# Performance work log

Measured on AMD Instinct MI355X. Metric: run time of the kernel, lower is better.

## Reference

```python
import jax, jax.numpy as jnp
import numpy as np

HEADS = 8
OUT_C = 8
NEG_SLOPE = 0.2  # PyG GATConv default


def setup_inputs() -> dict:
    key = jax.random.key(0)
    k = jax.random.split(key, 6)
    N, F, E = 100000, 128, 1600000
    x = jax.random.normal(k[0], (N, F), dtype=jnp.float32)
    edge_index = jax.random.randint(k[1], (2, E), 0, N, dtype=jnp.int64)
    W = jax.random.normal(k[2], (F, HEADS * OUT_C), dtype=jnp.float32) * (1.0 / np.sqrt(F))
    att_src = jax.random.normal(k[3], (HEADS, OUT_C), dtype=jnp.float32) * 0.1
    att_dst = jax.random.normal(k[4], (HEADS, OUT_C), dtype=jnp.float32) * 0.1
    bias = jnp.zeros((HEADS * OUT_C,), dtype=jnp.float32)
    return {"x": x, "edge_index": edge_index, "W": W,
            "att_src": att_src, "att_dst": att_dst, "bias": bias}


def reference(x, edge_index, W, att_src, att_dst, bias):
    N = x.shape[0]
    # add self loops (PyG default add_self_loops=True)
    loops = jnp.arange(N, dtype=edge_index.dtype)
    src = jnp.concatenate([edge_index[0], loops])  # [E']
    dst = jnp.concatenate([edge_index[1], loops])  # [E']

    h = (x @ W).reshape(N, HEADS, OUT_C)          # [N,H,C]
    a_src = jnp.einsum('nhc,hc->nh', h, att_src)  # [N,H]
    a_dst = jnp.einsum('nhc,hc->nh', h, att_dst)  # [N,H]

    # per-edge LeakyReLU attention logits
    e = jax.nn.leaky_relu(a_src[src] + a_dst[dst], NEG_SLOPE)  # [E',H]

    # segment softmax over incoming edges of each destination node
    emax = jax.ops.segment_max(e, dst, num_segments=N)  # every node has a self loop
    ex = jnp.exp(e - emax[dst])
    denom = jax.ops.segment_sum(ex, dst, num_segments=N)
    alpha = ex / denom[dst]  # [E',H]  (dropout on alpha skipped: eval mode)

    # scatter-add weighted source features
    out = jax.ops.segment_sum(alpha[:, :, None] * h[src], dst, num_segments=N)  # [N,H,C]
    return out.reshape(N, HEADS * OUT_C) + bias
```

## Files before the change

kernel.cpp:

```cpp
#include <hip/hip_runtime.h>
#include <hip/hip_bf16.h>


#define F 128
#define HC 64
#define H 8
#define NSLC 64

__device__ inline ushort f2bf(float f) {
    unsigned u = __float_as_uint(f);
    u += 0x7fff + ((u >> 16) & 1);
    return (ushort)(u >> 16);
}

__global__ __launch_bounds__(256) void k_gemm(const float* __restrict__ x,
                                              const float* __restrict__ W,
                                              const float* __restrict__ att_src,
                                              const float* __restrict__ att_dst,
                                              ushort* __restrict__ h2,
                                              float* __restrict__ a_src,
                                              float* __restrict__ a_dst, int N) {
    __shared__ float xs[64][F];
    const int tid  = threadIdx.x;
    const int row0 = blockIdx.x * 64;
    #pragma unroll
    for (int i = 0; i < 8; ++i) {
        int idx = i * 256 + tid;
        int r = idx >> 5;
        float4 v = make_float4(0.f, 0.f, 0.f, 0.f);
        if (row0 + r < N) v = ((const float4*)x)[(size_t)row0 * 32 + idx];
        ((float4*)xs)[idx] = v;
    }
    __syncthreads();
    const int c0 = (tid & 15) * 4;
    const int r0 = (tid >> 4) * 4;
    float acc[4][4] = {};
    for (int k = 0; k < F; k += 4) {
        float w[4][4];
        *(float4*)w[0] = *(const float4*)&W[(size_t)(k + 0) * HC + c0];
        *(float4*)w[1] = *(const float4*)&W[(size_t)(k + 1) * HC + c0];
        *(float4*)w[2] = *(const float4*)&W[(size_t)(k + 2) * HC + c0];
        *(float4*)w[3] = *(const float4*)&W[(size_t)(k + 3) * HC + c0];
        #pragma unroll
        for (int i = 0; i < 4; ++i) {
            float4 xv = *(const float4*)&xs[r0 + i][k];
            #pragma unroll
            for (int c = 0; c < 4; ++c) {
                acc[i][c] += xv.x * w[0][c];
                acc[i][c] += xv.y * w[1][c];
                acc[i][c] += xv.z * w[2][c];
                acc[i][c] += xv.w * w[3][c];
            }
        }
    }
    const int head = (tid & 15) >> 1;
    const int cb   = c0 & 7;
    float as4[4], ad4[4];
    #pragma unroll
    for (int c = 0; c < 4; ++c) {
        as4[c] = att_src[head * 8 + cb + c];
        ad4[c] = att_dst[head * 8 + cb + c];
    }
    #pragma unroll
    for (int i = 0; i < 4; ++i) {
        int r = row0 + r0 + i;
        if (r < N) {
            ushort4 pk;
            pk.x = f2bf(acc[i][0]); pk.y = f2bf(acc[i][1]);
            pk.z = f2bf(acc[i][2]); pk.w = f2bf(acc[i][3]);
            *(ushort4*)&h2[(size_t)r * HC + c0] = pk;
            float ps = acc[i][0]*as4[0] + acc[i][1]*as4[1] +
                       acc[i][2]*as4[2] + acc[i][3]*as4[3];
            float pd = acc[i][0]*ad4[0] + acc[i][1]*ad4[1] +
                       acc[i][2]*ad4[2] + acc[i][3]*ad4[3];
            ps += __shfl_xor(ps, 1);
            pd += __shfl_xor(pd, 1);
            if ((tid & 1) == 0) {
                a_src[(size_t)r * H + head] = ps;
                a_dst[(size_t)r * H + head] = pd;
            }
        }
    }
}

__global__ __launch_bounds__(1024) void k_h(const int* __restrict__ ei,
                                            ushort* __restrict__ hist,
                                            int E, int npg) {
    extern __shared__ int lcnt[];
    const int grp = blockIdx.x & 7;
    const int lo  = grp * npg;
    const unsigned len = (unsigned)npg;
    for (int i = threadIdx.x; i < npg; i += 1024) lcnt[i] = 0;
    __syncthreads();
    const int t    = (blockIdx.x >> 3) * 1024 + threadIdx.x;
    const int nthr = (gridDim.x >> 3) * 1024;
    const int a0 = (4 - (E & 3)) & 3;
    const int nv = (E - a0) >> 2;
    const int4* vd = (const int4*)(ei + E + a0);
    for (int q = t; q < nv; q += nthr) {
        int4 d = vd[q];
        unsigned c;
        c = (unsigned)(d.x - lo); if (c < len) atomicAdd(&lcnt[c], 1);
        c = (unsigned)(d.y - lo); if (c < len) atomicAdd(&lcnt[c], 1);
        c = (unsigned)(d.z - lo); if (c < len) atomicAdd(&lcnt[c], 1);
        c = (unsigned)(d.w - lo); if (c < len) atomicAdd(&lcnt[c], 1);
    }
    if (blockIdx.x < 8) {
        int r = (E - a0) & 3;
        int e = -1;
        int tx = (int)threadIdx.x;
        if (tx < a0) e = tx;
        else if (tx - a0 < r) e = a0 + (nv << 2) + (tx - a0);
        if (e >= 0) {
            unsigned c = (unsigned)(ei[E + e] - lo);
            if (c < len) atomicAdd(&lcnt[c], 1);
        }
    }
    __syncthreads();
    ushort* hrow = hist + (size_t)blockIdx.x * npg;
    for (int i = threadIdx.x; i < npg; i += 1024) hrow[i] = (ushort)lcnt[i];
}

__global__ __launch_bounds__(256) void k_scan1(const ushort* __restrict__ hist,
                                               int* __restrict__ offs,
                                               int* __restrict__ bsums,
                                               int N, int npg) {
    __shared__ int s[256];
    int i = blockIdx.x * 256 + threadIdx.x;
    int v = 0;
    if (i < N) {
        int g = i / npg;
        int c = i - g * npg;
        const ushort* hp = hist + (size_t)g * npg + c;
        #pragma unroll 8
        for (int j = 0; j < NSLC; ++j) v += hp[(size_t)(j << 3) * npg];
        v += 1;
    }
    s[threadIdx.x] = v;
    __syncthreads();
    for (int d = 1; d < 256; d <<= 1) {
        int t = (threadIdx.x >= d) ? s[threadIdx.x - d] : 0;
        __syncthreads();
        s[threadIdx.x] += t;
        __syncthreads();
    }
    if (i < N) offs[i] = s[threadIdx.x] - v;
    if (threadIdx.x == 255) bsums[blockIdx.x] = s[255];
}

__global__ __launch_bounds__(512) void k_scan2(int* __restrict__ bsums, int nb) {
    __shared__ int s[512];
    int v = (threadIdx.x < nb) ? bsums[threadIdx.x] : 0;
    s[threadIdx.x] = v;
    __syncthreads();
    for (int d = 1; d < 512; d <<= 1) {
        int t = (threadIdx.x >= d) ? s[threadIdx.x - d] : 0;
        __syncthreads();
        s[threadIdx.x] += t;
        __syncthreads();
    }
    if (threadIdx.x < nb) bsums[threadIdx.x] = s[threadIdx.x] - v;
}

__global__ __launch_bounds__(256) void k_scan3(int* __restrict__ offs,
                                               const int* __restrict__ bsums,
                                               ushort* __restrict__ hist,
                                               int* __restrict__ srcs,
                                               int N, int npg, int Etot) {
    int i = blockIdx.x * 256 + threadIdx.x;
    if (i == 0) offs[N] = Etot;
    if (i >= N) return;
    int o = offs[i] + bsums[i >> 8];
    offs[i] = o;
    srcs[o] = i;
    int g = i / npg;
    int c = i - g * npg;
    ushort* hp = hist + (size_t)g * npg + c;
    int p = 0;
    #pragma unroll 8
    for (int j = 0; j < NSLC; ++j) {
        size_t off = (size_t)(j << 3) * npg;
        int t = hp[off];
        hp[off] = (ushort)p;
        p += t;
    }
}

__global__ __launch_bounds__(1024) void k_scat(const int* __restrict__ ei,
                                               const ushort* __restrict__ hist,
                                               const int* __restrict__ offs,
                                               int* __restrict__ srcs,
                                               int E, int npg) {
    extern __shared__ int lpos[];
    const int grp = blockIdx.x & 7;
    const int lo  = grp * npg;
    const unsigned len = (unsigned)npg;
    const ushort* hrow = hist + (size_t)blockIdx.x * npg;
    for (int i = threadIdx.x; i < npg; i += 1024)
        lpos[i] = offs[lo + i] + 1 + (int)hrow[i];
    __syncthreads();
    const int t    = (blockIdx.x >> 3) * 1024 + threadIdx.x;
    const int nthr = (gridDim.x >> 3) * 1024;
    const int a0 = (4 - (E & 3)) & 3;
    const int nv = (E - a0) >> 2;
    const int4* vd = (const int4*)(ei + E + a0);
    for (int q = t; q < nv; q += nthr) {
        int4 d = vd[q];
        unsigned c0 = (unsigned)(d.x - lo), c1 = (unsigned)(d.y - lo),
                 c2 = (unsigned)(d.z - lo), c3 = (unsigned)(d.w - lo);
        if ((c0 < len) | (c1 < len) | (c2 < len) | (c3 < len)) {
            int e = a0 + (q << 2);
            if (c0 < len) { int p = atomicAdd(&lpos[c0], 1); srcs[p] = ei[e];     }
            if (c1 < len) { int p = atomicAdd(&lpos[c1], 1); srcs[p] = ei[e + 1]; }
            if (c2 < len) { int p = atomicAdd(&lpos[c2], 1); srcs[p] = ei[e + 2]; }
            if (c3 < len) { int p = atomicAdd(&lpos[c3], 1); srcs[p] = ei[e + 3]; }
        }
    }
    if (blockIdx.x < 8) {
        int r = (E - a0) & 3;
        int e = -1;
        int tx = (int)threadIdx.x;
        if (tx < a0) e = tx;
        else if (tx - a0 < r) e = a0 + (nv << 2) + (tx - a0);
        if (e >= 0) {
            unsigned c = (unsigned)(ei[E + e] - lo);
            if (c < len) { int p = atomicAdd(&lpos[c], 1); srcs[p] = ei[e]; }
        }
    }
}

__global__ __launch_bounds__(256) void k_gat(const int* __restrict__ offs,
                                             const int* __restrict__ srcs,
                                             const ushort* __restrict__ h2,
                                             const float* __restrict__ a_src,
                                             const float* __restrict__ a_dst,
                                             const float* __restrict__ bias,
                                             float* __restrict__ out, int N) {
    const int lane = threadIdx.x & 63;
    const int half = lane >> 5;
    const int l32  = lane & 31;
    const int g    = l32 >> 3;
    const int hd   = l32 & 7;
    const int wave = threadIdx.x >> 6;
    const int d = blockIdx.x * 8 + wave * 2 + half;
    const bool valid = d < N;

    int off = 0, end = 0;
    float adst = 0.f;
    if (valid) {
        off  = offs[d];
        end  = offs[d + 1];
        adst = a_dst[d * H + hd];
    }

    float acc[8] = {0.f, 0.f, 0.f, 0.f, 0.f, 0.f, 0.f, 0.f};
    float den = 0.f;

    for (int i = off + g; i < end; i += 8) {
        const int i2 = i + 4;
        const bool has1 = (i2 < end);
        int s0 = srcs[i];
        int s1 = has1 ? srcs[i2] : s0;
        float a0 = a_src[s0 * H + hd] + adst;
        float a1 = a_src[s1 * H + hd] + adst;
        a0 = a0 > 0.f ? a0 : 0.2f * a0;
        a1 = a1 > 0.f ? a1 : 0.2f * a1;
        float ex0 = __expf(a0);
        float ex1 = has1 ? __expf(a1) : 0.f;
        uint4 u0 = *(const uint4*)(h2 + ((size_t)s0 << 6) + (hd << 3));
        uint4 u1 = *(const uint4*)(h2 + ((size_t)s1 << 6) + (hd << 3));
        acc[0] += ex0 * __uint_as_float(u0.x << 16);
        acc[1] += ex0 * __uint_as_float(u0.x & 0xffff0000u);
        acc[2] += ex0 * __uint_as_float(u0.y << 16);
        acc[3] += ex0 * __uint_as_float(u0.y & 0xffff0000u);
        acc[4] += ex0 * __uint_as_float(u0.z << 16);
        acc[5] += ex0 * __uint_as_float(u0.z & 0xffff0000u);
        acc[6] += ex0 * __uint_as_float(u0.w << 16);
        acc[7] += ex0 * __uint_as_float(u0.w & 0xffff0000u);
        acc[0] += ex1 * __uint_as_float(u1.x << 16);
        acc[1] += ex1 * __uint_as_float(u1.x & 0xffff0000u);
        acc[2] += ex1 * __uint_as_float(u1.y << 16);
        acc[3] += ex1 * __uint_as_float(u1.y & 0xffff0000u);
        acc[4] += ex1 * __uint_as_float(u1.z << 16);
        acc[5] += ex1 * __uint_as_float(u1.z & 0xffff0000u);
        acc[6] += ex1 * __uint_as_float(u1.w << 16);
        acc[7] += ex1 * __uint_as_float(u1.w & 0xffff0000u);
        den += ex0 + ex1;
    }

    #pragma unroll
    for (int m = 8; m <= 16; m <<= 1) {
        #pragma unroll
        for (int c = 0; c < 8; ++c) acc[c] += __shfl_xor(acc[c], m);
        den += __shfl_xor(den, m);
    }

    if (g == 0 && valid) {
        float r = 1.f / den;
        float4 o0, o1;
        o0.x = acc[0]*r + bias[hd*8+0]; o0.y = acc[1]*r + bias[hd*8+1];
        o0.z = acc[2]*r + bias[hd*8+2]; o0.w = acc[3]*r + bias[hd*8+3];
        o1.x = acc[4]*r + bias[hd*8+4]; o1.y = acc[5]*r + bias[hd*8+5];
        o1.z = acc[6]*r + bias[hd*8+6]; o1.w = acc[7]*r + bias[hd*8+7];
        *(float4*)&out[(size_t)d * HC + hd * 8]     = o0;
        *(float4*)&out[(size_t)d * HC + hd * 8 + 4] = o1;
    }
}

extern "C" void kernel_launch(void* const* d_in, const int* in_sizes, int n_in,
                              void* d_out, int out_size, void* d_ws, size_t ws_size,
                              hipStream_t stream) {
    const float* x       = (const float*)d_in[0];
    const int*   ei      = (const int*)d_in[1];
    const float* W       = (const float*)d_in[2];
    const float* att_src = (const float*)d_in[3];
    const float* att_dst = (const float*)d_in[4];
    const float* bias    = (const float*)d_in[5];
    const int N = in_sizes[0] / F;
    const int E = in_sizes[1] / 2;
    const int Etot = E + N;
    const int npg = (N + 7) / 8;
    float* out = (float*)d_out;

    ushort* h2    = (ushort*)d_ws;
    float*  a_src = (float*)(h2 + (size_t)N * HC);
    float*  a_dst = a_src + (size_t)N * H;
    int*    offs  = (int*)(a_dst + (size_t)N * H);
    int*    bsums = offs + N + 1;
    ushort* hist  = (ushort*)(bsums + 512);
    int*    srcs  = (int*)(hist + (size_t)8 * NSLC * npg);

    const int nb = (N + 255) / 256;
    const size_t ldsz = (size_t)npg * sizeof(int);
    k_gemm <<<(N + 63) / 64, 256, 0, stream>>>(x, W, att_src, att_dst, h2, a_src, a_dst, N);
    k_h    <<<8 * NSLC, 1024, ldsz, stream>>>(ei, hist, E, npg);
    k_scan1<<<nb, 256, 0, stream>>>(hist, offs, bsums, N, npg);
    k_scan2<<<1, 512, 0, stream>>>(bsums, nb);
    k_scan3<<<nb, 256, 0, stream>>>(offs, bsums, hist, srcs, N, npg, Etot);
    k_scat <<<8 * NSLC, 1024, ldsz, stream>>>(ei, hist, offs, srcs, E, npg);
    k_gat  <<<(N + 7) / 8, 256, 0, stream>>>(offs, srcs, h2, a_src, a_dst, bias, out, N);
}
```

Measured before the change: 237.8 us.

## Pre-partition edges by destination group into packed payload before CSR histogram and scatter

Previously the histogram and scatter kernels each made every one of 8 group-blocks stream the entire destination array and filter for its own group, reading edge_index eight times over. The new path first counts edges per coarse destination group, scans those counts, and writes a packed (src<<14 | local dst) payload grouped by destination range. The histogram and scatter kernels then read only their own group's slice, and the slice count is halved. This adds three small kernels and an extra payload buffer. The packing assumes src fits in 18 bits and a local destination index fits in 14 bits, which holds for N=100000.

```diff
diff --git a/kernel.cpp b/kernel.cpp
--- a/kernel.cpp
+++ b/kernel.cpp
@@ -5,7 +5,8 @@
 #define F 128
 #define HC 64
 #define H 8
-#define NSLC 64
+#define NS 32
+#define PB 512
 
 __device__ inline ushort f2bf(float f) {
     unsigned u = __float_as_uint(f);
@@ -83,39 +84,121 @@
     }
 }
 
-__global__ __launch_bounds__(1024) void k_h(const int* __restrict__ ei,
-                                            ushort* __restrict__ hist,
-                                            int E, int npg) {
-    extern __shared__ int lcnt[];
-    const int grp = blockIdx.x & 7;
-    const int lo  = grp * npg;
-    const unsigned len = (unsigned)npg;
-    for (int i = threadIdx.x; i < npg; i += 1024) lcnt[i] = 0;
-    __syncthreads();
-    const int t    = (blockIdx.x >> 3) * 1024 + threadIdx.x;
-    const int nthr = (gridDim.x >> 3) * 1024;
+__device__ inline unsigned grp_of(int d, unsigned Mg) {
+    return (unsigned)(((unsigned long long)(unsigned)d * Mg) >> 32);
+}
+
+__global__ __launch_bounds__(256) void k_c(const int* __restrict__ ei,
+                                           int* __restrict__ pcntT,
+                                           int E, unsigned Mg) {
+    __shared__ int cnt[8];
+    if (threadIdx.x < 8) cnt[threadIdx.x] = 0;
+    __syncthreads();
+    const int t    = blockIdx.x * 256 + threadIdx.x;
+    const int nthr = PB * 256;
     const int a0 = (4 - (E & 3)) & 3;
     const int nv = (E - a0) >> 2;
     const int4* vd = (const int4*)(ei + E + a0);
     for (int q = t; q < nv; q += nthr) {
         int4 d = vd[q];
-        unsigned c;
-        c = (unsigned)(d.x - lo); if (c < len) atomicAdd(&lcnt[c], 1);
-        c = (unsigned)(d.y - lo); if (c < len) atomicAdd(&lcnt[c], 1);
-        c = (unsigned)(d.z - lo); if (c < len) atomicAdd(&lcnt[c], 1);
-        c = (unsigned)(d.w - lo); if (c < len) atomicAdd(&lcnt[c], 1);
-    }
-    if (blockIdx.x < 8) {
+        atomicAdd(&cnt[grp_of(d.x, Mg)], 1);
+        atomicAdd(&cnt[grp_of(d.y, Mg)], 1);
+        atomicAdd(&cnt[grp_of(d.z, Mg)], 1);
+        atomicAdd(&cnt[grp_of(d.w, Mg)], 1);
+    }
+    if (blockIdx.x == 0) {
+        int r = (E - a0) & 3;
+        int e = -1;
+        int tx = (int)threadIdx.x;
+        if (tx < a0) e = tx;
+        else if (tx - a0 < r) e = a0 + (nv << 2) + (tx - a0);
+        if (e >= 0) atomicAdd(&cnt[grp_of(ei[E + e], Mg)], 1);
+    }
+    __syncthreads();
+    if (threadIdx.x < 8) pcntT[(size_t)threadIdx.x * PB + blockIdx.x] = cnt[threadIdx.x];
+}
+
+__global__ __launch_bounds__(1024) void k_sA(int* __restrict__ pcntT,
+                                             int* __restrict__ gEdgeBase, int E) {
+    __shared__ int s[1024];
+    const int S2 = 8 * PB;
+    const int base = threadIdx.x * (S2 / 1024);
+    int v[4]; int sum = 0;
+    #pragma unroll
+    for (int k = 0; k < S2 / 1024; ++k) { v[k] = pcntT[base + k]; sum += v[k]; }
+    s[threadIdx.x] = sum;
+    __syncthreads();
+    for (int d = 1; d < 1024; d <<= 1) {
+        int t = (threadIdx.x >= d) ? s[threadIdx.x - d] : 0;
+        __syncthreads();
+        s[threadIdx.x] += t;
+        __syncthreads();
+    }
+    int run = s[threadIdx.x] - sum;
+    #pragma unroll
+    for (int k = 0; k < S2 / 1024; ++k) {
+        int idx = base + k;
+        pcntT[idx] = run;
+        if ((idx % PB) == 0) gEdgeBase[idx / PB] = run;
+        run += v[k];
+    }
+    if (threadIdx.x == 0) gEdgeBase[8] = E;
+}
+
+__global__ __launch_bounds__(256) void k_p(const int* __restrict__ ei,
+                                           const int* __restrict__ pcntT,
+                                           unsigned* __restrict__ payload,
+                                           int E, unsigned Mg, int npg) {
+    __shared__ int lpos[8];
+    if (threadIdx.x < 8) lpos[threadIdx.x] = pcntT[(size_t)threadIdx.x * PB + blockIdx.x];
+    __syncthreads();
+    const int t    = blockIdx.x * 256 + threadIdx.x;
+    const int nthr = PB * 256;
+    const int a0 = (4 - (E & 3)) & 3;
+    const int nv = (E - a0) >> 2;
+    const int4* vd = (const int4*)(ei + E + a0);
+    for (int q = t; q < nv; q += nthr) {
+        int4 d = vd[q];
+        int e = a0 + (q << 2);
+        int s0 = ei[e], s1 = ei[e + 1], s2 = ei[e + 2], s3 = ei[e + 3];
+        unsigned g; int pos;
+        g = grp_of(d.x, Mg); pos = atomicAdd(&lpos[g], 1);
+        payload[pos] = ((unsigned)s0 << 14) | (unsigned)(d.x - (int)g * npg);
+        g = grp_of(d.y, Mg); pos = atomicAdd(&lpos[g], 1);
+        payload[pos] = ((unsigned)s1 << 14) | (unsigned)(d.y - (int)g * npg);
+        g = grp_of(d.z, Mg); pos = atomicAdd(&lpos[g], 1);
+        payload[pos] = ((unsigned)s2 << 14) | (unsigned)(d.z - (int)g * npg);
+        g = grp_of(d.w, Mg); pos = atomicAdd(&lpos[g], 1);
+        payload[pos] = ((unsigned)s3 << 14) | (unsigned)(d.w - (int)g * npg);
+    }
+    if (blockIdx.x == 0) {
         int r = (E - a0) & 3;
         int e = -1;
         int tx = (int)threadIdx.x;
         if (tx < a0) e = tx;
         else if (tx - a0 < r) e = a0 + (nv << 2) + (tx - a0);
         if (e >= 0) {
-            unsigned c = (unsigned)(ei[E + e] - lo);
-            if (c < len) atomicAdd(&lcnt[c], 1);
+            int dv = ei[E + e];
+            unsigned g = grp_of(dv, Mg);
+            int pos = atomicAdd(&lpos[g], 1);
+            payload[pos] = ((unsigned)ei[e] << 14) | (unsigned)(dv - (int)g * npg);
         }
     }
+}
+
+__global__ __launch_bounds__(1024) void k_h2(const unsigned* __restrict__ payload,
+                                             const int* __restrict__ gEdgeBase,
+                                             ushort* __restrict__ hist, int npg) {
+    extern __shared__ int lcnt[];
+    const int g = blockIdx.x & 7, sl = blockIdx.x >> 3;
+    for (int i = threadIdx.x; i < npg; i += 1024) lcnt[i] = 0;
+    __syncthreads();
+    const int gb0 = gEdgeBase[g], gb1 = gEdgeBase[g + 1];
+    const int chunk = (gb1 - gb0 + NS - 1) / NS;
+    const int lo = gb0 + sl * chunk;
+    const int hi = min(lo + chunk, gb1);
+    for (int i = lo + threadIdx.x; i < hi; i += 1024)
+        atomicAdd(&lcnt[payload[i] & 16383u], 1);
     __syncthreads();
     ushort* hrow = hist + (size_t)blockIdx.x * npg;
     for (int i = threadIdx.x; i < npg; i += 1024) hrow[i] = (ushort)lcnt[i];
@@ -133,7 +216,7 @@
         int c = i - g * npg;
         const ushort* hp = hist + (size_t)g * npg + c;
         #pragma unroll 8
-        for (int j = 0; j < NSLC; ++j) v += hp[(size_t)(j << 3) * npg];
+        for (int j = 0; j < NS; ++j) v += hp[(size_t)(j << 3) * npg];
         v += 1;
     }
     s[threadIdx.x] = v;
@@ -178,7 +261,7 @@
     ushort* hp = hist + (size_t)g * npg + c;
     int p = 0;
     #pragma unroll 8
-    for (int j = 0; j < NSLC; ++j) {
+    for (int j = 0; j < NS; ++j) {
         size_t off = (size_t)(j << 3) * npg;
         int t = hp[off];
         hp[off] = (ushort)p;
@@ -186,46 +269,28 @@
     }
 }
 
-__global__ __launch_bounds__(1024) void k_scat(const int* __restrict__ ei,
-                                               const ushort* __restrict__ hist,
-                                               const int* __restrict__ offs,
-                                               int* __restrict__ srcs,
-                                               int E, int npg) {
+__global__ __launch_bounds__(1024) void k_scat2(const unsigned* __restrict__ payload,
+                                                const int* __restrict__ gEdgeBase,
+                                                const ushort* __restrict__ hist,
+                                                const int* __restrict__ offs,
+                                                int* __restrict__ srcs,
+                                                int npg, int N) {
     extern __shared__ int lpos[];
-    const int grp = blockIdx.x & 7;
-    const int lo  = grp * npg;
-    const unsigned len = (unsigned)npg;
+    const int g = blockIdx.x & 7, sl = blockIdx.x >> 3;
+    const int lod = g * npg;
+    const int len = min(npg, N - lod);
     const ushort* hrow = hist + (size_t)blockIdx.x * npg;
-    for (int i = threadIdx.x; i < npg; i += 1024)
-        lpos[i] = offs[lo + i] + 1 + (int)hrow[i];
-    __syncthreads();
-    const int t    = (blockIdx.x >> 3) * 1024 + threadIdx.x;
-    const int nthr = (gridDim.x >> 3) * 1024;
-    const int a0 = (4 - (E & 3)) & 3;
-    const int nv = (E - a0) >> 2;
-    const int4* vd = (const int4*)(ei + E + a0);
-    for (int q = t; q < nv; q += nthr) {
-        int4 d = vd[q];
-        unsigned c0 = (unsigned)(d.x - lo), c1 = (unsigned)(d.y - lo),
-                 c2 = (unsigned)(d.z - lo), c3 = (unsigned)(d.w - lo);
-        if ((c0 < len) | (c1 < len) | (c2 < len) | (c3 < len)) {
-            int e = a0 + (q << 2);
-            if (c0 < len) { int p = atomicAdd(&lpos[c0], 1); srcs[p] = ei[e];     }
-            if (c1 < len) { int p = atomicAdd(&lpos[c1], 1); srcs[p] = ei[e + 1]; }
-            if (c2 < len) { int p = atomicAdd(&lpos[c2], 1); srcs[p] = ei[e + 2]; }
-            if (c3 < len) { int p = atomicAdd(&lpos[c3], 1); srcs[p] = ei[e + 3]; }
-        }
-    }
-    if (blockIdx.x < 8) {
-        int r = (E - a0) & 3;
-        int e = -1;
-        int tx = (int)threadIdx.x;
-        if (tx < a0) e = tx;
-        else if (tx - a0 < r) e = a0 + (nv << 2) + (tx - a0);
-        if (e >= 0) {
-            unsigned c = (unsigned)(ei[E + e] - lo);
-            if (c < len) { int p = atomicAdd(&lpos[c], 1); srcs[p] = ei[e]; }
-        }
+    for (int i = threadIdx.x; i < len; i += 1024)
+        lpos[i] = offs[lod + i] + 1 + (int)hrow[i];
+    __syncthreads();
+    const int gb0 = gEdgeBase[g], gb1 = gEdgeBase[g + 1];
+    const int chunk = (gb1 - gb0 + NS - 1) / NS;
+    const int lo = gb0 + sl * chunk;
+    const int hi = min(lo + chunk, gb1);
+    for (int i = lo + threadIdx.x; i < hi; i += 1024) {
+        unsigned p = payload[i];
+        int pos = atomicAdd(&lpos[p & 16383u], 1);
+        srcs[pos] = (int)(p >> 14);
     }
 }
 
@@ -320,23 +385,31 @@
     const int E = in_sizes[1] / 2;
     const int Etot = E + N;
     const int npg = (N + 7) / 8;
+    const unsigned Mg = (unsigned)(((1ULL << 32) + (unsigned)npg - 1) / (unsigned)npg);
     float* out = (float*)d_out;
 
-    ushort* h2    = (ushort*)d_ws;
-    float*  a_src = (float*)(h2 + (size_t)N * HC);
-    float*  a_dst = a_src + (size_t)N * H;
-    int*    offs  = (int*)(a_dst + (size_t)N * H);
-    int*    bsums = offs + N + 1;
-    ushort* hist  = (ushort*)(bsums + 512);
-    int*    srcs  = (int*)(hist + (size_t)8 * NSLC * npg);
+    ushort*   h2      = (ushort*)d_ws;
+    float*    a_src   = (float*)(h2 + (size_t)N * HC);
+    float*    a_dst   = a_src + (size_t)N * H;
+    int*      offs    = (int*)(a_dst + (size_t)N * H);
+    int*      bsums   = offs + N + 1;
+    int*      pcntT   = bsums + 512;
+    int*      gEdgeBase = pcntT + 8 * PB;
+    ushort*   hist    = (ushort*)(gEdgeBase + 16);
+    size_t    histE   = ((size_t)8 * NS * npg + 3) & ~(size_t)3;
+    unsigned* payload = (unsigned*)(hist + histE);
+    int*      srcs    = (int*)(payload + E);
 
     const int nb = (N + 255) / 256;
     const size_t ldsz = (size_t)npg * sizeof(int);
     k_gemm <<<(N + 63) / 64, 256, 0, stream>>>(x, W, att_src, att_dst, h2, a_src, a_dst, N);
-    k_h    <<<8 * NSLC, 1024, ldsz, stream>>>(ei, hist, E, npg);
+    k_c    <<<PB, 256, 0, stream>>>(ei, pcntT, E, Mg);
+    k_sA   <<<1, 1024, 0, stream>>>(pcntT, gEdgeBase, E);
+    k_p    <<<PB, 256, 0, stream>>>(ei, pcntT, payload, E, Mg, npg);
+    k_h2   <<<8 * NS, 1024, ldsz, stream>>>(payload, gEdgeBase, hist, npg);
     k_scan1<<<nb, 256, 0, stream>>>(hist, offs, bsums, N, npg);
     k_scan2<<<1, 512, 0, stream>>>(bsums, nb);
     k_scan3<<<nb, 256, 0, stream>>>(offs, bsums, hist, srcs, N, npg, Etot);
-    k_scat <<<8 * NSLC, 1024, ldsz, stream>>>(ei, hist, offs, srcs, E, npg);
+    k_scat2<<<8 * NS, 1024, ldsz, stream>>>(payload, gEdgeBase, hist, offs, srcs, npg, N);
     k_gat  <<<(N + 7) / 8, 256, 0, stream>>>(offs, srcs, h2, a_src, a_dst, bias, out, N);
 }
```

Measured after the change: 224.2 us. -5.7%, faster.

## Fuse CSR build into one cooperative kernel with two-level bucketed partitioning

Applied to the files above, without the earlier changes.

Replaces the five histogram, scan and scatter kernels with a single cooperative kernel that uses grid-wide syncs. Edges are first partitioned into 8 destination groups and packed as (src<<14 | local dst) payloads, so the per-group histogram and scatter passes read only their own bucket instead of rescanning every edge 8 times. This cuts launch overhead and redundant edge reads, at the cost of an extra payload buffer, a bit-packing scheme that assumes src fits in 18 bits and local dst in 14 bits, and five grid barriers.

```diff
diff --git a/kernel.cpp b/kernel.cpp
--- a/kernel.cpp
+++ b/kernel.cpp
@@ -1,11 +1,16 @@
 #include <hip/hip_runtime.h>
 #include <hip/hip_bf16.h>
+#include <hip/hip_cooperative_groups.h>
 
 
 #define F 128
 #define HC 64
 #define H 8
-#define NSLC 64
+#define NG 8
+#define NSB 256
+#define NS 32
+
+namespace cg = cooperative_groups;
 
 __device__ inline ushort f2bf(float f) {
     unsigned u = __float_as_uint(f);
@@ -83,148 +88,183 @@
     }
 }
 
-__global__ __launch_bounds__(1024) void k_h(const int* __restrict__ ei,
-                                            ushort* __restrict__ hist,
-                                            int E, int npg) {
-    extern __shared__ int lcnt[];
-    const int grp = blockIdx.x & 7;
-    const int lo  = grp * npg;
-    const unsigned len = (unsigned)npg;
-    for (int i = threadIdx.x; i < npg; i += 1024) lcnt[i] = 0;
-    __syncthreads();
-    const int t    = (blockIdx.x >> 3) * 1024 + threadIdx.x;
-    const int nthr = (gridDim.x >> 3) * 1024;
+__device__ inline unsigned grp_of(int d, unsigned Mg) {
+    return (unsigned)(((unsigned long long)(unsigned)d * Mg) >> 32);
+}
+
+__global__ __launch_bounds__(1024) void k_build(const int* __restrict__ ei,
+                                                int* __restrict__ pcntT,
+                                                unsigned* __restrict__ payload,
+                                                ushort* __restrict__ hist,
+                                                int* __restrict__ offs,
+                                                int* __restrict__ bsums,
+                                                int* __restrict__ srcs,
+                                                int E, int N, int npg,
+                                                unsigned Mg, int Etot) {
+    extern __shared__ int lds[];
+    cg::grid_group grid = cg::this_grid();
+    const int t  = threadIdx.x;
+    const int b  = blockIdx.x;
+    const int g  = b & (NG - 1);
+    const int sl = b >> 3;
+
     const int a0 = (4 - (E & 3)) & 3;
     const int nv = (E - a0) >> 2;
     const int4* vd = (const int4*)(ei + E + a0);
-    for (int q = t; q < nv; q += nthr) {
+    const int t0   = b * 1024 + t;
+    const int nthr = NSB * 1024;
+
+    if (t < NG) lds[t] = 0;
+    __syncthreads();
+    for (int q = t0; q < nv; q += nthr) {
         int4 d = vd[q];
-        unsigned c;
-        c = (unsigned)(d.x - lo); if (c < len) atomicAdd(&lcnt[c], 1);
-        c = (unsigned)(d.y - lo); if (c < len) atomicAdd(&lcnt[c], 1);
-        c = (unsigned)(d.z - lo); if (c < len) atomicAdd(&lcnt[c], 1);
-        c = (unsigned)(d.w - lo); if (c < len) atomicAdd(&lcnt[c], 1);
-    }
-    if (blockIdx.x < 8) {
+        atomicAdd(&lds[grp_of(d.x, Mg)], 1);
+        atomicAdd(&lds[grp_of(d.y, Mg)], 1);
+        atomicAdd(&lds[grp_of(d.z, Mg)], 1);
+        atomicAdd(&lds[grp_of(d.w, Mg)], 1);
+    }
+    if (b == 0) {
         int r = (E - a0) & 3;
         int e = -1;
-        int tx = (int)threadIdx.x;
-        if (tx < a0) e = tx;
-        else if (tx - a0 < r) e = a0 + (nv << 2) + (tx - a0);
-        if (e >= 0) {
-            unsigned c = (unsigned)(ei[E + e] - lo);
-            if (c < len) atomicAdd(&lcnt[c], 1);
-        }
-    }
-    __syncthreads();
-    ushort* hrow = hist + (size_t)blockIdx.x * npg;
-    for (int i = threadIdx.x; i < npg; i += 1024) hrow[i] = (ushort)lcnt[i];
-}
-
-__global__ __launch_bounds__(256) void k_scan1(const ushort* __restrict__ hist,
-                                               int* __restrict__ offs,
-                                               int* __restrict__ bsums,
-                                               int N, int npg) {
-    __shared__ int s[256];
-    int i = blockIdx.x * 256 + threadIdx.x;
-    int v = 0;
-    if (i < N) {
-        int g = i / npg;
-        int c = i - g * npg;
-        const ushort* hp = hist + (size_t)g * npg + c;
-        #pragma unroll 8
-        for (int j = 0; j < NSLC; ++j) v += hp[(size_t)(j << 3) * npg];
-        v += 1;
-    }
-    s[threadIdx.x] = v;
-    __syncthreads();
-    for (int d = 1; d < 256; d <<= 1) {
-        int t = (threadIdx.x >= d) ? s[threadIdx.x - d] : 0;
-        __syncthreads();
-        s[threadIdx.x] += t;
-        __syncthreads();
-    }
-    if (i < N) offs[i] = s[threadIdx.x] - v;
-    if (threadIdx.x == 255) bsums[blockIdx.x] = s[255];
-}
-
-__global__ __launch_bounds__(512) void k_scan2(int* __restrict__ bsums, int nb) {
-    __shared__ int s[512];
-    int v = (threadIdx.x < nb) ? bsums[threadIdx.x] : 0;
-    s[threadIdx.x] = v;
-    __syncthreads();
-    for (int d = 1; d < 512; d <<= 1) {
-        int t = (threadIdx.x >= d) ? s[threadIdx.x - d] : 0;
-        __syncthreads();
-        s[threadIdx.x] += t;
-        __syncthreads();
-    }
-    if (threadIdx.x < nb) bsums[threadIdx.x] = s[threadIdx.x] - v;
-}
-
-__global__ __launch_bounds__(256) void k_scan3(int* __restrict__ offs,
-                                               const int* __restrict__ bsums,
-                                               ushort* __restrict__ hist,
-                                               int* __restrict__ srcs,
-                                               int N, int npg, int Etot) {
-    int i = blockIdx.x * 256 + threadIdx.x;
-    if (i == 0) offs[N] = Etot;
-    if (i >= N) return;
-    int o = offs[i] + bsums[i >> 8];
-    offs[i] = o;
-    srcs[o] = i;
-    int g = i / npg;
-    int c = i - g * npg;
-    ushort* hp = hist + (size_t)g * npg + c;
-    int p = 0;
-    #pragma unroll 8
-    for (int j = 0; j < NSLC; ++j) {
-        size_t off = (size_t)(j << 3) * npg;
-        int t = hp[off];
-        hp[off] = (ushort)p;
-        p += t;
-    }
-}
-
-__global__ __launch_bounds__(1024) void k_scat(const int* __restrict__ ei,
-                                               const ushort* __restrict__ hist,
-                                               const int* __restrict__ offs,
-                                               int* __restrict__ srcs,
-                                               int E, int npg) {
-    extern __shared__ int lpos[];
-    const int grp = blockIdx.x & 7;
-    const int lo  = grp * npg;
-    const unsigned len = (unsigned)npg;
-    const ushort* hrow = hist + (size_t)blockIdx.x * npg;
-    for (int i = threadIdx.x; i < npg; i += 1024)
-        lpos[i] = offs[lo + i] + 1 + (int)hrow[i];
-    __syncthreads();
-    const int t    = (blockIdx.x >> 3) * 1024 + threadIdx.x;
-    const int nthr = (gridDim.x >> 3) * 1024;
-    const int a0 = (4 - (E & 3)) & 3;
-    const int nv = (E - a0) >> 2;
-    const int4* vd = (const int4*)(ei + E + a0);
-    for (int q = t; q < nv; q += nthr) {
+        if (t < a0) e = t;
+        else if (t - a0 < r) e = a0 + (nv << 2) + (t - a0);
+        if (e >= 0) atomicAdd(&lds[grp_of(ei[E + e], Mg)], 1);
+    }
+    __syncthreads();
+    if (t < NG) pcntT[t * NSB + b] = lds[t];
+    grid.sync();
+
+    int v0 = pcntT[2 * t], v1 = pcntT[2 * t + 1];
+    int psum = v0 + v1;
+    lds[2048 + t] = psum;
+    __syncthreads();
+    for (int dd = 1; dd < 1024; dd <<= 1) {
+        int tmp = (t >= dd) ? lds[2048 + t - dd] : 0;
+        __syncthreads();
+        lds[2048 + t] += tmp;
+        __syncthreads();
+    }
+    int excl = lds[2048 + t] - psum;
+    lds[2 * t] = excl;
+    lds[2 * t + 1] = excl + v0;
+    __syncthreads();
+    const int gb0 = lds[g * NSB];
+    const int gb1 = (g == NG - 1) ? E : lds[(g + 1) * NSB];
+    if (t < NG) lds[3072 + t] = lds[t * NSB + b];
+    __syncthreads();
+    for (int q = t0; q < nv; q += nthr) {
         int4 d = vd[q];
-        unsigned c0 = (unsigned)(d.x - lo), c1 = (unsigned)(d.y - lo),
-                 c2 = (unsigned)(d.z - lo), c3 = (unsigned)(d.w - lo);
-        if ((c0 < len) | (c1 < len) | (c2 < len) | (c3 < len)) {
-            int e = a0 + (q << 2);
-            if (c0 < len) { int p = atomicAdd(&lpos[c0], 1); srcs[p] = ei[e];     }
-            if (c1 < len) { int p = atomicAdd(&lpos[c1], 1); srcs[p] = ei[e + 1]; }
-            if (c2 < len) { int p = atomicAdd(&lpos[c2], 1); srcs[p] = ei[e + 2]; }
-            if (c3 < len) { int p = atomicAdd(&lpos[c3], 1); srcs[p] = ei[e + 3]; }
-        }
-    }
-    if (blockIdx.x < 8) {
+        int e = a0 + (q << 2);
+        int s0 = ei[e], s1 = ei[e + 1], s2 = ei[e + 2], s3 = ei[e + 3];
+        unsigned gg; int pos;
+        gg = grp_of(d.x, Mg); pos = atomicAdd(&lds[3072 + gg], 1);
+        payload[pos] = ((unsigned)s0 << 14) | (unsigned)(d.x - (int)gg * npg);
+        gg = grp_of(d.y, Mg); pos = atomicAdd(&lds[3072 + gg], 1);
+        payload[pos] = ((unsigned)s1 << 14) | (unsigned)(d.y - (int)gg * npg);
+        gg = grp_of(d.z, Mg); pos = atomicAdd(&lds[3072 + gg], 1);
+        payload[pos] = ((unsigned)s2 << 14) | (unsigned)(d.z - (int)gg * npg);
+        gg = grp_of(d.w, Mg); pos = atomicAdd(&lds[3072 + gg], 1);
+        payload[pos] = ((unsigned)s3 << 14) | (unsigned)(d.w - (int)gg * npg);
+    }
+    if (b == 0) {
         int r = (E - a0) & 3;
         int e = -1;
-        int tx = (int)threadIdx.x;
-        if (tx < a0) e = tx;
-        else if (tx - a0 < r) e = a0 + (nv << 2) + (tx - a0);
+        if (t < a0) e = t;
+        else if (t - a0 < r) e = a0 + (nv << 2) + (t - a0);
         if (e >= 0) {
-            unsigned c = (unsigned)(ei[E + e] - lo);
-            if (c < len) { int p = atomicAdd(&lpos[c], 1); srcs[p] = ei[e]; }
+            int dv = ei[E + e];
+            unsigned gg = grp_of(dv, Mg);
+            int pos = atomicAdd(&lds[3072 + gg], 1);
+            payload[pos] = ((unsigned)ei[e] << 14) | (unsigned)(dv - (int)gg * npg);
+        }
+    }
+    grid.sync();
+
+    for (int i = t; i < npg; i += 1024) lds[i] = 0;
+    __syncthreads();
+    {
+        const int chunk = (gb1 - gb0 + NS - 1) / NS;
+        const int lo = gb0 + sl * chunk;
+        const int hi = min(lo + chunk, gb1);
+        for (int i = lo + t; i < hi; i += 1024)
+            atomicAdd(&lds[payload[i] & 16383u], 1);
+    }
+    __syncthreads();
+    {
+        ushort* hrow = hist + (size_t)b * npg;
+        for (int i = t; i < npg; i += 1024) hrow[i] = (ushort)lds[i];
+    }
+    grid.sync();
+
+    const int GD = (N + NSB - 1) / NSB;
+    const int di = b * GD + t;
+    int dv2 = 0;
+    if (t < GD && di < N) {
+        unsigned gg = grp_of(di, Mg);
+        int c = di - (int)gg * npg;
+        const ushort* hp = hist + (size_t)gg * npg + c;
+        #pragma unroll 8
+        for (int j = 0; j < NS; ++j) dv2 += hp[(size_t)(j << 3) * npg];
+        dv2 += 1;
+    }
+    if (t < 512) lds[t] = (t < GD) ? dv2 : 0;
+    __syncthreads();
+    for (int dd = 1; dd < 512; dd <<= 1) {
+        int tmp = 0;
+        if (t < 512 && t >= dd) tmp = lds[t - dd];
+        __syncthreads();
+        if (t < 512) lds[t] += tmp;
+        __syncthreads();
+    }
+    if (t < GD) lds[512 + t] = lds[t] - dv2;
+    if (t == 0) bsums[b] = lds[511];
+    grid.sync();
+
+    int bv = 0;
+    if (t < NSB) { bv = bsums[t]; lds[1024 + t] = bv; }
+    __syncthreads();
+    for (int dd = 1; dd < NSB; dd <<= 1) {
+        int tmp = 0;
+        if (t < NSB && t >= dd) tmp = lds[1024 + t - dd];
+        __syncthreads();
+        if (t < NSB) lds[1024 + t] += tmp;
+        __syncthreads();
+    }
+    if (t < NSB) lds[1280 + t] = lds[1024 + t] - bv;
+    __syncthreads();
+    const int base = lds[1280 + b];
+    if (b == 0 && t == 0) offs[N] = Etot;
+    if (t < GD && di < N) {
+        int o = lds[512 + t] + base;
+        offs[di] = o;
+        srcs[o] = di;
+        unsigned gg = grp_of(di, Mg);
+        int c = di - (int)gg * npg;
+        ushort* hp = hist + (size_t)gg * npg + c;
+        int p = 0;
+        #pragma unroll 8
+        for (int j = 0; j < NS; ++j) {
+            size_t off = (size_t)(j << 3) * npg;
+            int tt = hp[off];
+            hp[off] = (ushort)p;
+            p += tt;
+        }
+    }
+    grid.sync();
+
+    {
+        const int lod = g * npg;
+        const ushort* hrow = hist + (size_t)b * npg;
+        for (int i = t; i < npg; i += 1024)
+            lds[i] = offs[lod + i] + 1 + (int)hrow[i];
+        __syncthreads();
+        const int chunk = (gb1 - gb0 + NS - 1) / NS;
+        const int lo = gb0 + sl * chunk;
+        const int hi = min(lo + chunk, gb1);
+        for (int i = lo + t; i < hi; i += 1024) {
+            unsigned p = payload[i];
+            int pos = atomicAdd(&lds[p & 16383u], 1);
+            srcs[pos] = (int)(p >> 14);
         }
     }
 }
@@ -316,27 +356,31 @@
     const float* att_src = (const float*)d_in[3];
     const float* att_dst = (const float*)d_in[4];
     const float* bias    = (const float*)d_in[5];
-    const int N = in_sizes[0] / F;
-    const int E = in_sizes[1] / 2;
-    const int Etot = E + N;
-    const int npg = (N + 7) / 8;
+    int N = in_sizes[0] / F;
+    int E = in_sizes[1] / 2;
+    int Etot = E + N;
+    int npg = (N + NG - 1) / NG;
+    unsigned Mg = (unsigned)(((1ULL << 32) + (unsigned)npg - 1) / (unsigned)npg);
     float* out = (float*)d_out;
 
-    ushort* h2    = (ushort*)d_ws;
-    float*  a_src = (float*)(h2 + (size_t)N * HC);
-    float*  a_dst = a_src + (size_t)N * H;
-    int*    offs  = (int*)(a_dst + (size_t)N * H);
-    int*    bsums = offs + N + 1;
-    ushort* hist  = (ushort*)(bsums + 512);
-    int*    srcs  = (int*)(hist + (size_t)8 * NSLC * npg);
-
-    const int nb = (N + 255) / 256;
-    const size_t ldsz = (size_t)npg * sizeof(int);
-    k_gemm <<<(N + 63) / 64, 256, 0, stream>>>(x, W, att_src, att_dst, h2, a_src, a_dst, N);
-    k_h    <<<8 * NSLC, 1024, ldsz, stream>>>(ei, hist, E, npg);
-    k_scan1<<<nb, 256, 0, stream>>>(hist, offs, bsums, N, npg);
-    k_scan2<<<1, 512, 0, stream>>>(bsums, nb);
-    k_scan3<<<nb, 256, 0, stream>>>(offs, bsums, hist, srcs, N, npg, Etot);
-    k_scat <<<8 * NSLC, 1024, ldsz, stream>>>(ei, hist, offs, srcs, E, npg);
-    k_gat  <<<(N + 7) / 8, 256, 0, stream>>>(offs, srcs, h2, a_src, a_dst, bias, out, N);
-}
+    ushort*   h2      = (ushort*)d_ws;
+    float*    a_src   = (float*)(h2 + (size_t)N * HC);
+    float*    a_dst   = a_src + (size_t)N * H;
+    int*      offs    = (int*)(a_dst + (size_t)N * H);
+    int*      bsums   = offs + N + 1;
+    int*      pcntT   = bsums + NSB;
+    ushort*   hist    = (ushort*)(pcntT + NG * NSB);
+    size_t    histE   = ((size_t)NSB * npg + 3) & ~(size_t)3;
+    unsigned* payload = (unsigned*)(hist + histE);
+    int*      srcs    = (int*)(payload + E);
+
+    const int* eic = ei;
+    void* args[] = {(void*)&eic, (void*)&pcntT, (void*)&payload, (void*)&hist,
+                    (void*)&offs, (void*)&bsums, (void*)&srcs,
+                    (void*)&E, (void*)&N, (void*)&npg, (void*)&Mg, (void*)&Etot};
+
+    k_gemm<<<(N + 63) / 64, 256, 0, stream>>>(x, W, att_src, att_dst, h2, a_src, a_dst, N);
+    hipLaunchCooperativeKernel((const void*)k_build, dim3(NSB), dim3(1024),
+                               args, 50000, stream);
+    k_gat <<<(N + 7) / 8, 256, 0, stream>>>(offs, srcs, h2, a_src, a_dst, bias, out, N);
+}
```

Result: slower. 375.4 us (+57.9%).
